# Optimization experiments

Measured on AMD Instinct MI355X. Metric: run time of the kernel, lower is better.

Reference implementation:

```python
import jax, jax.numpy as jnp
import numpy as np

B, N_SRC, N_TGT = 2, 2048, 2048
DIM, HEADS, DIM_HEAD, DIM_ROT = 1024, 16, 64, 32
INNER = HEADS * DIM_HEAD
SCALE = DIM_HEAD ** -0.5


def rotate_every_two(x):
    # (..., d) with d even: pairs (x1, x2) -> (-x2, x1), interleaved
    x1 = x[..., ::2]
    x2 = x[..., 1::2]
    return jnp.stack((-x2, x1), axis=-1).reshape(x.shape)


def setup_inputs() -> dict:
    key = jax.random.key(0)
    ks = jax.random.split(key, 10)
    return {
        "src": jax.random.normal(ks[0], (B, N_SRC, DIM), jnp.float32),
        "sin_src": jax.random.uniform(ks[1], (B, N_SRC, DIM_ROT), jnp.float32, -1.0, 1.0),
        "cos_src": jax.random.uniform(ks[2], (B, N_SRC, DIM_ROT), jnp.float32, -1.0, 1.0),
        "tgt": jax.random.normal(ks[3], (B, N_TGT, DIM), jnp.float32),
        "sin_tgt": jax.random.uniform(ks[4], (B, N_TGT, DIM_ROT), jnp.float32, -1.0, 1.0),
        "cos_tgt": jax.random.uniform(ks[5], (B, N_TGT, DIM_ROT), jnp.float32, -1.0, 1.0),
        "wq": jax.random.normal(ks[6], (DIM, INNER), jnp.float32) / np.sqrt(DIM),
        "wkv": jax.random.normal(ks[7], (DIM, 2 * INNER), jnp.float32) / np.sqrt(DIM),
        "wout": jax.random.normal(ks[8], (INNER, DIM), jnp.float32) / np.sqrt(INNER),
        "bout": jnp.zeros((DIM,), jnp.float32),
    }


def reference(src, sin_src, cos_src, tgt, sin_tgt, cos_tgt, wq, wkv, wout, bout):
    b = src.shape[0]
    q = tgt @ wq                                  # (b, i, inner)
    k, v = jnp.split(src @ wkv, 2, axis=-1)       # (b, j, inner) each

    def split_heads(t):
        return t.reshape(b, t.shape[1], HEADS, DIM_HEAD).transpose(0, 2, 1, 3)

    q, k, v = map(split_heads, (q, k, v))          # (b, h, n, d)

    # rotary on leading DIM_ROT dims; pos embs broadcast across heads
    st, ct = sin_tgt[:, None], cos_tgt[:, None]    # (b, 1, i, dr)
    ss, cs = sin_src[:, None], cos_src[:, None]    # (b, 1, j, dr)
    q_rot, q_pass = q[..., :DIM_ROT], q[..., DIM_ROT:]
    k_rot, k_pass = k[..., :DIM_ROT], k[..., DIM_ROT:]
    q_rot = q_rot * ct + rotate_every_two(q_rot) * st
    k_rot = k_rot * cs + rotate_every_two(k_rot) * ss
    q = jnp.concatenate([q_rot, q_pass], axis=-1)
    k = jnp.concatenate([k_rot, k_pass], axis=-1)

    dots = jnp.einsum('bhid,bhjd->bhij', q, k) * SCALE
    attn = jax.nn.softmax(dots, axis=-1)
    out = jnp.einsum('bhij,bhjd->bhid', attn, v)
    out = out.transpose(0, 2, 1, 3).reshape(b, out.shape[2], INNER)
    return out @ wout + bout, attn
```

## Files before the change

kernel.cpp:

```cpp
#include <hip/hip_runtime.h>
#include <hip/hip_bf16.h>
#include <cstdint>
#include <cstddef>

#define NB 2
#define NSEQ 2048
#define NHEADS 16
#define HD 64
#define DMODEL 1024
#define SCALEF 0.125f

typedef __attribute__((ext_vector_type(4))) float f32x4;
typedef __attribute__((ext_vector_type(8))) short s16x8;

__device__ __forceinline__ unsigned short f2bf(float f) {
  union { float f; unsigned u; } v; v.f = f;
  unsigned u = v.u;
  return (unsigned short)((u + 0x7fffu + ((u >> 16) & 1u)) >> 16);
}
__device__ __forceinline__ float bf2f(unsigned short s) {
  union { unsigned u; float f; } v; v.u = ((unsigned)s) << 16;
  return v.f;
}

__global__ void k_convert2(const float* __restrict__ a, const float* __restrict__ b,
                           unsigned short* __restrict__ oa, unsigned short* __restrict__ ob) {
  int bx = blockIdx.x;
  const float* in = (bx < 4096) ? a : b;
  unsigned short* out = (bx < 4096) ? oa : ob;
  int i = (bx & 4095) * 256 + threadIdx.x;
  float4 v = ((const float4*)in)[i];
  ushort4 o;
  o.x = f2bf(v.x); o.y = f2bf(v.y); o.z = f2bf(v.z); o.w = f2bf(v.w);
  ((ushort4*)out)[i] = o;
}

__global__ void k_transpose_all(const float* __restrict__ wq, unsigned short* __restrict__ wq_t,
                                const float* __restrict__ wkv, unsigned short* __restrict__ wkv_t,
                                const float* __restrict__ wout, unsigned short* __restrict__ wout_t) {
  const int z = blockIdx.z;
  const float* w; unsigned short* wt; int N;
  if (z == 0)      { w = wq;   wt = wq_t;   N = 1024; }
  else if (z == 1) { w = wkv;  wt = wkv_t;  N = 2048; }
  else             { w = wout; wt = wout_t; N = 1024; }
  if (blockIdx.x * 64 >= N) return;
  __shared__ float t[64][65];
  int n0 = blockIdx.x * 64, k0 = blockIdx.y * 64;
  int c = threadIdx.x & 63, rb = threadIdx.x >> 6;
#pragma unroll
  for (int rr = 0; rr < 16; rr++) {
    int k = rb * 16 + rr;
    t[c][k] = w[(size_t)(k0 + k) * N + n0 + c];
  }
  __syncthreads();
#pragma unroll
  for (int rr = 0; rr < 16; rr++) {
    int n = rb * 16 + rr;
    wt[(size_t)(n0 + n) * 1024 + k0 + c] = f2bf(t[n][c]);
  }
}

#define GLD16(gp, lp) __builtin_amdgcn_global_load_lds( \
    (const __attribute__((address_space(1))) unsigned int*)(gp), \
    (__attribute__((address_space(3))) unsigned int*)(lp), 16, 0, 0)

#define GEMM_BODY(A, Bt)                                                        \
  __shared__ unsigned short As[128 * 32];                                       \
  __shared__ unsigned short Bs[128 * 32];                                       \
  const int tid = threadIdx.x;                                                  \
  const int lane = tid & 63, wid = tid >> 6;                                    \
  const int m0 = blockIdx.y * 128, n0 = blockIdx.x * 128;                       \
  const int wr = wid >> 1, wc = wid & 1;                                        \
  const int lr = lane >> 2, l4 = lane & 3;                                      \
  const int lc = lane & 15, lg = lane >> 4;                                     \
  const unsigned short* pa0 = A + (size_t)(m0 + wid * 32 + lr) * 1024 + l4 * 8; \
  const unsigned short* pa1 = pa0 + (size_t)16 * 1024;                          \
  const unsigned short* pb0 = Bt + (size_t)(n0 + wid * 32 + lr) * 1024 + l4 * 8;\
  const unsigned short* pb1 = pb0 + (size_t)16 * 1024;                          \
  f32x4 acc[4][4] = {};                                                         \
  for (int kt = 0; kt < 1024; kt += 32) {                                       \
    GLD16(pa0 + kt, &As[wid * 1024]);                                           \
    GLD16(pa1 + kt, &As[wid * 1024 + 512]);                                     \
    GLD16(pb0 + kt, &Bs[wid * 1024]);                                           \
    GLD16(pb1 + kt, &Bs[wid * 1024 + 512]);                                     \
    __syncthreads();                                                            \
    s16x8 af[4], bfr[4];                                                        \
    _Pragma("unroll")                                                           \
    for (int m = 0; m < 4; m++)                                                 \
      af[m] = *(const s16x8*)&As[(wr * 64 + m * 16 + lc) * 32 + lg * 8];        \
    _Pragma("unroll")                                                           \
    for (int n = 0; n < 4; n++)                                                 \
      bfr[n] = *(const s16x8*)&Bs[(wc * 64 + n * 16 + lc) * 32 + lg * 8];       \
    __builtin_amdgcn_s_setprio(1);                                              \
    _Pragma("unroll")                                                           \
    for (int m = 0; m < 4; m++)                                                 \
      _Pragma("unroll")                                                         \
      for (int n = 0; n < 4; n++)                                               \
        acc[m][n] = __builtin_amdgcn_mfma_f32_16x16x32_bf16(af[m], bfr[n], acc[m][n], 0, 0, 0); \
    __builtin_amdgcn_s_setprio(0);                                              \
    __syncthreads();                                                            \
  }

__global__ __launch_bounds__(256) void k_gemm(const unsigned short* __restrict__ A,
                                              const unsigned short* __restrict__ Bt,
                                              float* __restrict__ C,
                                              const float* __restrict__ bias) {
  GEMM_BODY(A, Bt)
  float bv[4];
#pragma unroll
  for (int n = 0; n < 4; n++) bv[n] = bias[n0 + wc * 64 + n * 16 + lc];
#pragma unroll
  for (int m = 0; m < 4; m++) {
#pragma unroll
    for (int n = 0; n < 4; n++) {
      int col = n0 + wc * 64 + n * 16 + lc;
#pragma unroll
      for (int r = 0; r < 4; r++) {
        int row = m0 + wr * 64 + m * 16 + lg * 4 + r;
        C[(size_t)row * 1024 + col] = acc[m][n][r] + bv[n];
      }
    }
  }
}

__global__ __launch_bounds__(256) void k_gemmq(const unsigned short* __restrict__ A,
                                               const unsigned short* __restrict__ Bt,
                                               const float* __restrict__ sinp,
                                               const float* __restrict__ cosp,
                                               unsigned short* __restrict__ qhb) {
  GEMM_BODY(A, Bt)
#pragma unroll
  for (int m = 0; m < 4; m++) {
#pragma unroll
    for (int n = 0; n < 4; n++) {
      int c = n0 + wc * 64 + n * 16 + lc;
      int h = c >> 6, d = c & 63;
      bool dorope = (d < 32);
#pragma unroll
      for (int r = 0; r < 4; r++) {
        int row = m0 + wr * 64 + m * 16 + lg * 4 + r;
        float x = acc[m][n][r];
        float px = __shfl_xor(x, 1);
        float o = x;
        if (dorope) {
          float s = sinp[(size_t)row * 32 + d];
          float cz = cosp[(size_t)row * 32 + d];
          o = (d & 1) ? (x * cz + px * s) : (x * cz - px * s);
        }
        int b = row >> 11, i = row & 2047;
        qhb[((size_t)(b * NHEADS + h) * NSEQ + i) * HD + d] = f2bf(o);
      }
    }
  }
}

__global__ __launch_bounds__(256) void k_gemmkv(const unsigned short* __restrict__ A,
                                                const unsigned short* __restrict__ Bt,
                                                const float* __restrict__ sinp,
                                                const float* __restrict__ cosp,
                                                unsigned short* __restrict__ khb,
                                                unsigned short* __restrict__ vtb) {
  GEMM_BODY(A, Bt)
#pragma unroll
  for (int m = 0; m < 4; m++) {
#pragma unroll
    for (int n = 0; n < 4; n++) {
      int c = n0 + wc * 64 + n * 16 + lc;
      int d = c & 63;
      if (c < 1024) {
        int h = c >> 6;
        bool dorope = (d < 32);
#pragma unroll
        for (int r = 0; r < 4; r++) {
          int row = m0 + wr * 64 + m * 16 + lg * 4 + r;
          float x = acc[m][n][r];
          float px = __shfl_xor(x, 1);
          float o = x;
          if (dorope) {
            float s = sinp[(size_t)row * 32 + d];
            float cz = cosp[(size_t)row * 32 + d];
            o = (d & 1) ? (x * cz + px * s) : (x * cz - px * s);
          }
          int b = row >> 11, i = row & 2047;
          khb[((size_t)(b * NHEADS + h) * NSEQ + i) * HD + d] = f2bf(o);
        }
      } else {
        int h = (c - 1024) >> 6;
#pragma unroll
        for (int r = 0; r < 4; r++) (void)__shfl_xor(acc[m][n][r], 1);
        ushort4 o;
        o.x = f2bf(acc[m][n][0]); o.y = f2bf(acc[m][n][1]);
        o.z = f2bf(acc[m][n][2]); o.w = f2bf(acc[m][n][3]);
        int row0 = m0 + wr * 64 + m * 16 + lg * 4;
        int b = row0 >> 11, i = row0 & 2047;
        *(ushort4*)&vtb[((size_t)(b * NHEADS + h) * HD + d) * NSEQ + i] = o;
      }
    }
  }
}

#define QBLK 32
#define SROWB 2056
__global__ __launch_bounds__(1024, 4) void k_attn(const unsigned short* __restrict__ qh,
                                                  const unsigned short* __restrict__ kh,
                                                  const unsigned short* __restrict__ vt,
                                                  float* __restrict__ attn_g,
                                                  unsigned short* __restrict__ ctx) {
  __shared__ unsigned short Sbf[QBLK * SROWB];
  __shared__ float wred[16][32];
  __shared__ float invr[32];
  float* part = (float*)Sbf;

  const int tid = threadIdx.x;
  const int lane = tid & 63, wid = tid >> 6;
  const int i0 = blockIdx.x * QBLK;
  const int h = blockIdx.y, b = blockIdx.z;
  const int lc = lane & 15, lg = lane >> 4;
  const int wcb = wid * 128;

  const unsigned short* qb = qh + ((size_t)(b * NHEADS + h) * NSEQ + i0) * HD;
  const unsigned short* kb = kh + (size_t)(b * NHEADS + h) * NSEQ * HD;
  const unsigned short* vb = vt + (size_t)(b * NHEADS + h) * HD * NSEQ;

  s16x8 aq[2][2];
#pragma unroll
  for (int rg = 0; rg < 2; rg++) {
    aq[rg][0] = *(const s16x8*)&qb[(rg * 16 + lc) * HD + lg * 8];
    aq[rg][1] = *(const s16x8*)&qb[(rg * 16 + lc) * HD + 32 + lg * 8];
  }
  float psum[2][4] = {};
  const unsigned short* krow = kb + (size_t)(wcb + lc) * HD + lg * 8;
  s16x8 kp[2][2];
  kp[0][0] = *(const s16x8*)&krow[0];
  kp[0][1] = *(const s16x8*)&krow[32];
#pragma unroll
  for (int jf = 0; jf < 8; jf++) {
    if (jf < 7) {
      kp[(jf + 1) & 1][0] = *(const s16x8*)&krow[(size_t)((jf + 1) * 16) * HD];
      kp[(jf + 1) & 1][1] = *(const s16x8*)&krow[(size_t)((jf + 1) * 16) * HD + 32];
    }
    int j = wcb + jf * 16;
#pragma unroll
    for (int rg = 0; rg < 2; rg++) {
      f32x4 acc = {};
      acc = __builtin_amdgcn_mfma_f32_16x16x32_bf16(aq[rg][0], kp[jf & 1][0], acc, 0, 0, 0);
      acc = __builtin_amdgcn_mfma_f32_16x16x32_bf16(aq[rg][1], kp[jf & 1][1], acc, 0, 0, 0);
#pragma unroll
      for (int r = 0; r < 4; r++) {
        float e = __expf(acc[r] * SCALEF);
        psum[rg][r] += e;
        Sbf[(size_t)(rg * 16 + lg * 4 + r) * SROWB + j + lc] = f2bf(e);
      }
    }
  }
#pragma unroll
  for (int off = 1; off <= 8; off <<= 1)
#pragma unroll
    for (int rg = 0; rg < 2; rg++)
#pragma unroll
      for (int r = 0; r < 4; r++) psum[rg][r] += __shfl_xor(psum[rg][r], off);
  if (lc == 0) {
#pragma unroll
    for (int rg = 0; rg < 2; rg++)
#pragma unroll
      for (int r = 0; r < 4; r++) wred[wid][rg * 16 + lg * 4 + r] = psum[rg][r];
  }
  __syncthreads();
  if (tid < 32) {
    float tot = 0.f;
#pragma unroll
    for (int w = 0; w < 16; w++) tot += wred[w][tid];
    invr[tid] = 1.0f / tot;
  }

  f32x4 accd[2][4] = {};
  const unsigned short* vrow = vb + (size_t)lc * NSEQ + wcb + lg * 8;
  s16x8 vp[2][4];
#pragma unroll
  for (int f = 0; f < 4; f++)
    vp[0][f] = *(const s16x8*)&vrow[(size_t)(f * 16) * NSEQ];
#pragma unroll
  for (int jj = 0; jj < 4; jj++) {
    if (jj < 3) {
#pragma unroll
      for (int f = 0; f < 4; f++)
        vp[(jj + 1) & 1][f] = *(const s16x8*)&vrow[(size_t)(f * 16) * NSEQ + (jj + 1) * 32];
    }
    int jb = wcb + jj * 32;
    s16x8 af0 = *(const s16x8*)&Sbf[(size_t)lc * SROWB + jb + lg * 8];
    __builtin_amdgcn_s_setprio(1);
#pragma unroll
    for (int f = 0; f < 4; f++)
      accd[0][f] = __builtin_amdgcn_mfma_f32_16x16x32_bf16(af0, vp[jj & 1][f], accd[0][f], 0, 0, 0);
    __builtin_amdgcn_s_setprio(0);
    s16x8 af1 = *(const s16x8*)&Sbf[(size_t)(16 + lc) * SROWB + jb + lg * 8];
    __builtin_amdgcn_s_setprio(1);
#pragma unroll
    for (int f = 0; f < 4; f++)
      accd[1][f] = __builtin_amdgcn_mfma_f32_16x16x32_bf16(af1, vp[jj & 1][f], accd[1][f], 0, 0, 0);
    __builtin_amdgcn_s_setprio(0);
  }
  __syncthreads();

  {
    const int srow = tid >> 5;
    const int scc = (tid & 31) * 8;
    const float inv = invr[srow];
    float* arow = attn_g + ((size_t)(b * NHEADS + h) * NSEQ + i0 + srow) * NSEQ + scc;
#pragma unroll
    for (int k = 0; k < 8; k++) {
      s16x8 ev = *(const s16x8*)&Sbf[(size_t)srow * SROWB + scc + k * 256];
      f32x4 f0, f1;
      f0[0] = bf2f((unsigned short)ev[0]) * inv;
      f0[1] = bf2f((unsigned short)ev[1]) * inv;
      f0[2] = bf2f((unsigned short)ev[2]) * inv;
      f0[3] = bf2f((unsigned short)ev[3]) * inv;
      f1[0] = bf2f((unsigned short)ev[4]) * inv;
      f1[1] = bf2f((unsigned short)ev[5]) * inv;
      f1[2] = bf2f((unsigned short)ev[6]) * inv;
      f1[3] = bf2f((unsigned short)ev[7]) * inv;
      *(f32x4*)&arow[k * 256] = f0;
      *(f32x4*)&arow[k * 256 + 4] = f1;
    }
  }
  __syncthreads();

  if (wid < 8) {
#pragma unroll
    for (int rg = 0; rg < 2; rg++)
#pragma unroll
      for (int f = 0; f < 4; f++)
#pragma unroll
        for (int r = 0; r < 4; r++)
          part[((size_t)wid * 32 + rg * 16 + lg * 4 + r) * 65 + f * 16 + lc] = accd[rg][f][r];
  }
  __syncthreads();
  if (wid >= 8) {
#pragma unroll
    for (int rg = 0; rg < 2; rg++)
#pragma unroll
      for (int f = 0; f < 4; f++)
#pragma unroll
        for (int r = 0; r < 4; r++)
          part[((size_t)(wid - 8) * 32 + rg * 16 + lg * 4 + r) * 65 + f * 16 + lc] += accd[rg][f][r];
  }
  __syncthreads();

  {
    const int oi = tid >> 5;
    const int d0 = (tid & 31) * 2;
    float s0 = 0.f, s1 = 0.f;
#pragma unroll
    for (int p = 0; p < 8; p++) {
      s0 += part[((size_t)p * 32 + oi) * 65 + d0];
      s1 += part[((size_t)p * 32 + oi) * 65 + d0 + 1];
    }
    float iv = invr[oi];
    ushort2 o;
    o.x = f2bf(s0 * iv);
    o.y = f2bf(s1 * iv);
    *(ushort2*)&ctx[(size_t)(b * NSEQ + i0 + oi) * DMODEL + h * HD + d0] = o;
  }
}

extern "C" void kernel_launch(void* const* d_in, const int* in_sizes, int n_in,
                              void* d_out, int out_size, void* d_ws, size_t ws_size,
                              hipStream_t stream) {
  const float* src     = (const float*)d_in[0];
  const float* sin_src = (const float*)d_in[1];
  const float* cos_src = (const float*)d_in[2];
  const float* tgt     = (const float*)d_in[3];
  const float* sin_tgt = (const float*)d_in[4];
  const float* cos_tgt = (const float*)d_in[5];
  const float* wq      = (const float*)d_in[6];
  const float* wkv     = (const float*)d_in[7];
  const float* wout    = (const float*)d_in[8];
  const float* bout    = (const float*)d_in[9];

  if (ws_size < (size_t)109051904) return;

  uint8_t* w = (uint8_t*)d_ws;
  unsigned short* tgt_bf = (unsigned short*)(w + 0);
  unsigned short* src_bf = (unsigned short*)(w + 8388608);
  unsigned short* wq_t   = (unsigned short*)(w + 16777216);
  unsigned short* wkv_t  = (unsigned short*)(w + 18874368);
  unsigned short* wout_t = (unsigned short*)(w + 23068672);
  unsigned short* qhb    = (unsigned short*)(w + 75497472);
  unsigned short* khb    = (unsigned short*)(w + 83886080);
  unsigned short* vtb    = (unsigned short*)(w + 92274688);
  unsigned short* ctx    = (unsigned short*)(w + 100663296);

  float* out_p  = (float*)d_out;
  float* attn_p = out_p + (size_t)NB * NSEQ * DMODEL;

  k_convert2<<<8192, 256, 0, stream>>>(tgt, src, tgt_bf, src_bf);
  k_transpose_all<<<dim3(32, 16, 3), 256, 0, stream>>>(wq, wq_t, wkv, wkv_t, wout, wout_t);

  k_gemmq <<<dim3(8, 32),  256, 0, stream>>>(tgt_bf, wq_t,  sin_tgt, cos_tgt, qhb);
  k_gemmkv<<<dim3(16, 32), 256, 0, stream>>>(src_bf, wkv_t, sin_src, cos_src, khb, vtb);

  k_attn<<<dim3(64, 16, 2), 1024, 0, stream>>>(qhb, khb, vtb, attn_p, ctx);

  k_gemm<<<dim3(8, 32), 256, 0, stream>>>(ctx, wout_t, out_p, bout);
}
```

Before: 358.8 us.

## Interleave attention-probability stores with PV MFMA loop and remap block order

The normalized attention-matrix write-out, formerly a separate phase after the PV accumulation, is now interleaved into the PV loop, so global fp32 stores overlap with MFMA work. A barrier is added after the row-sum reduction so the inverse sums are visible earlier. The grid is flattened to 1D with head/batch in the low bits, so consecutive blocks cover different heads for the same query tile, which changes K/V cache locality. The interleaving may add register pressure and store-queue contention during the matrix-core loop.

```diff
diff --git a/kernel.cpp b/kernel.cpp
--- a/kernel.cpp
+++ b/kernel.cpp
@@ -213,8 +213,10 @@
 
   const int tid = threadIdx.x;
   const int lane = tid & 63, wid = tid >> 6;
-  const int i0 = blockIdx.x * QBLK;
-  const int h = blockIdx.y, b = blockIdx.z;
+  const int bid = blockIdx.x;
+  const int g = bid & 31, t = bid >> 5;
+  const int h = g & 15, b = g >> 4;
+  const int i0 = t * QBLK;
   const int lc = lane & 15, lg = lane >> 4;
   const int wcb = wid * 128;
 
@@ -272,6 +274,12 @@
     for (int w = 0; w < 16; w++) tot += wred[w][tid];
     invr[tid] = 1.0f / tot;
   }
+  __syncthreads();
+
+  const int srow = tid >> 5;
+  const int scc = (tid & 31) * 8;
+  const float sinv = invr[srow];
+  float* arow = attn_g + ((size_t)(b * NHEADS + h) * NSEQ + i0 + srow) * NSEQ + scc;
 
   f32x4 accd[2][4] = {};
   const unsigned short* vrow = vb + (size_t)lc * NSEQ + wcb + lg * 8;
@@ -299,26 +307,19 @@
     for (int f = 0; f < 4; f++)
       accd[1][f] = __builtin_amdgcn_mfma_f32_16x16x32_bf16(af1, vp[jj & 1][f], accd[1][f], 0, 0, 0);
     __builtin_amdgcn_s_setprio(0);
-  }
-  __syncthreads();
-
-  {
-    const int srow = tid >> 5;
-    const int scc = (tid & 31) * 8;
-    const float inv = invr[srow];
-    float* arow = attn_g + ((size_t)(b * NHEADS + h) * NSEQ + i0 + srow) * NSEQ + scc;
-#pragma unroll
-    for (int k = 0; k < 8; k++) {
+#pragma unroll
+    for (int kk = 0; kk < 2; kk++) {
+      int k = jj * 2 + kk;
       s16x8 ev = *(const s16x8*)&Sbf[(size_t)srow * SROWB + scc + k * 256];
       f32x4 f0, f1;
-      f0[0] = bf2f((unsigned short)ev[0]) * inv;
-      f0[1] = bf2f((unsigned short)ev[1]) * inv;
-      f0[2] = bf2f((unsigned short)ev[2]) * inv;
-      f0[3] = bf2f((unsigned short)ev[3]) * inv;
-      f1[0] = bf2f((unsigned short)ev[4]) * inv;
-      f1[1] = bf2f((unsigned short)ev[5]) * inv;
-      f1[2] = bf2f((unsigned short)ev[6]) * inv;
-      f1[3] = bf2f((unsigned short)ev[7]) * inv;
+      f0[0] = bf2f((unsigned short)ev[0]) * sinv;
+      f0[1] = bf2f((unsigned short)ev[1]) * sinv;
+      f0[2] = bf2f((unsigned short)ev[2]) * sinv;
+      f0[3] = bf2f((unsigned short)ev[3]) * sinv;
+      f1[0] = bf2f((unsigned short)ev[4]) * sinv;
+      f1[1] = bf2f((unsigned short)ev[5]) * sinv;
+      f1[2] = bf2f((unsigned short)ev[6]) * sinv;
+      f1[3] = bf2f((unsigned short)ev[7]) * sinv;
       *(f32x4*)&arow[k * 256] = f0;
       *(f32x4*)&arow[k * 256 + 4] = f1;
     }
@@ -399,7 +400,7 @@
   k_gemmq <<<dim3(8, 32),  256, 0, stream>>>(tgt_bf, wq_t,  sin_tgt, cos_tgt, qhb);
   k_gemmkv<<<dim3(16, 32), 256, 0, stream>>>(src_bf, wkv_t, sin_src, cos_src, khb, vtb);
 
-  k_attn<<<dim3(64, 16, 2), 1024, 0, stream>>>(qhb, khb, vtb, attn_p, ctx);
+  k_attn<<<2048, 1024, 0, stream>>>(qhb, khb, vtb, attn_p, ctx);
 
   k_gemm<<<dim3(8, 32), 256, 0, stream>>>(ctx, wout_t, out_p, bout);
 }
```

New measurement: 337.8 us. 1.06x faster.
